# Optimization experiments

Hardware: AMD Instinct MI355X
Metric: run time of the kernel (lower is better)

The kernel has to match this reference:

```python
import jax, jax.numpy as jnp
import numpy as np

S, B, D = 2048, 2, 1024
H, DH = 16, 64  # heads, dim_head; H*DH == D (required by out.view)
SCALE = DH ** -0.5


def setup_inputs() -> dict:
    key = jax.random.key(0)
    ks = jax.random.split(key, 9)
    s = 0.02
    return {
        "x": jax.random.normal(ks[0], (S, B, D), jnp.float32),
        "Wq": jax.random.normal(ks[1], (H * DH, D), jnp.float32) * s,
        "bq": jax.random.normal(ks[2], (H * DH,), jnp.float32) * s,
        "Wk": jax.random.normal(ks[3], (H * DH, D), jnp.float32) * s,
        "bk": jax.random.normal(ks[4], (H * DH,), jnp.float32) * s,
        "Wv": jax.random.normal(ks[5], (H * DH, D), jnp.float32) * s,
        "bv": jax.random.normal(ks[6], (H * DH,), jnp.float32) * s,
        "Wo": jax.random.normal(ks[7], (D, H * DH), jnp.float32) * s,
        "bo": jax.random.normal(ks[8], (D,), jnp.float32) * s,
    }


def reference(x, Wq, bq, Wk, bk, Wv, bv, Wo, bo):
    # x: [S, B, D] (seq-first, matching the torch module)
    q = (x @ Wq.T + bq).reshape(S, B, H, DH)
    k = (x @ Wk.T + bk).reshape(S, B, H, DH)
    v = (x @ Wv.T + bv).reshape(S, B, H, DH)
    # scores: [B, H, S, S]
    dots = jnp.einsum("sbhd,tbhd->bhst", q, k) * SCALE
    attn = jax.nn.softmax(dots, axis=-1)  # dropout p=0.0 -> identity
    out = jnp.einsum("bhst,tbhd->sbhd", attn, v).reshape(S, B, H * DH)
    return out @ Wo.T + bo
```

## Files before the change

### kernel.cpp

```cpp
#include <hip/hip_runtime.h>
#include <hip/hip_bf16.h>

typedef unsigned short u16;
typedef unsigned int u32;
typedef __bf16 bf16x8 __attribute__((ext_vector_type(8)));
typedef float f32x4 __attribute__((ext_vector_type(4)));
typedef float f32x16 __attribute__((ext_vector_type(16)));

static constexpr int kS = 2048;
static constexpr int kB = 2;
static constexpr int kD = 1024;
static constexpr int kDH = 64;
static constexpr int kM = kS * kB;
static constexpr float kScale = 0.125f;
static constexpr float kLog2e = 1.44269504088896340736f;

__device__ __forceinline__ u16 f2bf(float f) {
  return __builtin_bit_cast(u16, static_cast<__bf16>(f));
}

__device__ __forceinline__ u32 pack2(float lo, float hi) {
  union { u16 h[2]; u32 u; } x;
  x.h[0] = f2bf(lo); x.h[1] = f2bf(hi);
  return x.u;
}

__device__ __forceinline__ void permswap(u32& a, u32& b) {
  asm volatile("v_permlane32_swap_b32 %0, %1" : "+v"(a), "+v"(b));
}

__device__ __forceinline__ float exp2_hw(float x) {
  float r;
  asm("v_exp_f32 %0, %1" : "=v"(r) : "v"(x));
  return r;
}

__device__ __forceinline__ void load_lds16(const void* g, void* l) {
  __builtin_amdgcn_global_load_lds(
      (const __attribute__((address_space(1))) void*)g,
      (__attribute__((address_space(3))) void*)l, 16, 0, 0);
}

__global__ void cast_f32_bf16(const float* __restrict__ in, u16* __restrict__ out, int n) {
  int i = (blockIdx.x * blockDim.x + threadIdx.x) * 4;
  const int stride = gridDim.x * blockDim.x * 4;
  for (; i < n; i += stride) {
    const float4 v = *reinterpret_cast<const float4*>(in + i);
    ushort4 o;
    o.x = f2bf(v.x); o.y = f2bf(v.y); o.z = f2bf(v.z); o.w = f2bf(v.w);
    *reinterpret_cast<ushort4*>(out + i) = o;
  }
}

__global__ void cast_w4(const float* __restrict__ Wq, const float* __restrict__ Wk,
                        const float* __restrict__ Wv, const float* __restrict__ Wo,
                        u16* __restrict__ dq, u16* __restrict__ dk,
                        u16* __restrict__ dv, u16* __restrict__ dw) {
  const float* src; u16* dst;
  switch (blockIdx.y) {
    case 0: src = Wq; dst = dq; break;
    case 1: src = Wk; dst = dk; break;
    case 2: src = Wv; dst = dv; break;
    default: src = Wo; dst = dw; break;
  }
  const int i = (blockIdx.x * blockDim.x + threadIdx.x) * 4;
  const float4 v = *reinterpret_cast<const float4*>(src + i);
  ushort4 o;
  o.x = f2bf(v.x); o.y = f2bf(v.y); o.z = f2bf(v.z); o.w = f2bf(v.w);
  *reinterpret_cast<ushort4*>(dst + i) = o;
}

template <int MODE>
__device__ __forceinline__ void gemm_body(
    const u16* __restrict__ A, const u16* __restrict__ W,
    const float* __restrict__ bias, void* __restrict__ Out,
    int M, int N, int K, float oscale) {
  __shared__ u16 As[128 * 32];
  __shared__ u16 Bs[128 * 32];
  const int tid = threadIdx.x;
  const int lane = tid & 63;
  const int wid = tid >> 6;
  const int wr = (wid >> 1) * 64;
  const int wc = (wid & 1) * 64;
  const int l15 = lane & 15;
  const int lg = lane >> 4;
  const int tm = blockIdx.x * 128;
  const int tn = blockIdx.y * 128;

  f32x4 acc[4][4] = {};

  for (int k0 = 0; k0 < K; k0 += 32) {
#pragma unroll
    for (int p = 0; p < 2; ++p) {
      const int c = p * 256 + tid;
      const int row = c >> 2;
      const int cc = c & 3;
      load_lds16(A + (size_t)(tm + row) * K + k0 + cc * 8, &As[c * 8]);
      load_lds16(W + (size_t)(tn + row) * K + k0 + cc * 8, &Bs[c * 8]);
    }
    __syncthreads();
    bf16x8 af[4], bw[4];
#pragma unroll
    for (int i = 0; i < 4; ++i) {
      af[i] = *reinterpret_cast<const bf16x8*>(&As[(wr + i * 16 + l15) * 32 + lg * 8]);
      bw[i] = *reinterpret_cast<const bf16x8*>(&Bs[(wc + i * 16 + l15) * 32 + lg * 8]);
    }
#pragma unroll
    for (int i = 0; i < 4; ++i)
#pragma unroll
      for (int j = 0; j < 4; ++j)
        acc[i][j] = __builtin_amdgcn_mfma_f32_16x16x32_bf16(af[i], bw[j], acc[i][j], 0, 0, 0);
    __syncthreads();
  }

#pragma unroll
  for (int i = 0; i < 4; ++i)
#pragma unroll
    for (int j = 0; j < 4; ++j)
#pragma unroll
      for (int r = 0; r < 4; ++r) {
        const int row = tm + wr + i * 16 + lg * 4 + r;
        const int col = tn + wc + j * 16 + l15;
        const float v = (acc[i][j][r] + bias[col]) * oscale;
        if constexpr (MODE == 0) {
          reinterpret_cast<u16*>(Out)[(size_t)row * N + col] = f2bf(v);
        } else if constexpr (MODE == 1) {
          reinterpret_cast<float*>(Out)[(size_t)row * N + col] = v;
        } else {
          const int s_ = row >> 1, b_ = row & 1;
          const int h_ = col >> 6, dh_ = col & 63;
          reinterpret_cast<u16*>(Out)[((size_t)(b_ * 16 + h_) * 64 + dh_) * kS + s_] = f2bf(v);
        }
      }
}

__global__ __launch_bounds__(256) void qkv_gemm(
    const u16* __restrict__ xb,
    const u16* __restrict__ Wqb, const u16* __restrict__ Wkb, const u16* __restrict__ Wvb,
    const float* __restrict__ bq, const float* __restrict__ bk, const float* __restrict__ bv,
    u16* __restrict__ Q, u16* __restrict__ K, u16* __restrict__ Vt) {
  const int z = blockIdx.z;
  if (z == 2) {
    gemm_body<2>(xb, Wvb, bv, Vt, kM, kD, kD, 1.0f);
  } else if (z == 0) {
    gemm_body<0>(xb, Wqb, bq, Q, kM, kD, kD, kScale * kLog2e);
  } else {
    gemm_body<0>(xb, Wkb, bk, K, kM, kD, kD, 1.0f);
  }
}

__global__ __launch_bounds__(256) void out_gemm(
    const u16* __restrict__ Ob, const u16* __restrict__ Wob,
    const float* __restrict__ bo, float* __restrict__ out) {
  gemm_body<1>(Ob, Wob, bo, out, kM, kD, kD, 1.0f);
}

__global__ __launch_bounds__(512, 4) void attn_fwd(
    const u16* __restrict__ Qg, const u16* __restrict__ Kg,
    const u16* __restrict__ Vtg, u16* __restrict__ Og) {
  __shared__ u16 Ksm[2][2][64 * 64];
  __shared__ u16 Vsm[2][2][64 * 64];

  const int tid = threadIdx.x;
  const int lane = tid & 63;
  const int w = tid >> 6;
  const int half = w >> 2;
  const int wsub = w & 3;
  const int ltid = tid & 255;
  const int l31 = lane & 31;
  const int hi = lane >> 5;

  const int bid = blockIdx.x;
  const int xcd = bid & 7;
  const int idx = bid >> 3;
  const int bh = xcd * 4 + (idx & 3);
  const int qb = idx >> 2;
  const int b = bh & 1;
  const int h = bh >> 1;
  const int hoff = h * kDH;
  const int vslot = b * 16 + h;
  const int qrow = qb * 128 + wsub * 32 + l31;

  bf16x8 qf[4];
#pragma unroll
  for (int ks = 0; ks < 4; ++ks)
    qf[ks] = *reinterpret_cast<const bf16x8*>(
        &Qg[(size_t)(qrow * kB + b) * kD + hoff + ks * 16 + hi * 8]);

  f32x16 acc[2] = {};
  float lac[4] = {0.f, 0.f, 0.f, 0.f};

  auto stage = [&](int t0, int buf) {
#pragma unroll
    for (int p = 0; p < 2; ++p) {
      const int c = p * 256 + ltid;
      const int row = c >> 3;
      const int cc = c & 7;
      const int scc = cc ^ (row & 7);
      load_lds16(&Kg[(size_t)((t0 + row) * kB + b) * kD + hoff + scc * 8],
                 &Ksm[half][buf][c * 8]);
      load_lds16(&Vtg[(size_t)(vslot * 64 + row) * kS + t0 + scc * 8],
                 &Vsm[half][buf][c * 8]);
    }
  };

  const int tbase = half * 16;
  stage(tbase * 64, 0);

#pragma unroll 1
  for (int ti = 0; ti < 16; ++ti) {
    asm volatile("s_waitcnt vmcnt(0)" ::: "memory");
    __builtin_amdgcn_sched_barrier(0);
    __builtin_amdgcn_s_barrier();
    __builtin_amdgcn_sched_barrier(0);
    if (ti + 1 < 16) stage((tbase + ti + 1) * 64, (ti + 1) & 1);

    const int cur = ti & 1;

    f32x16 sc[2] = {};
    __builtin_amdgcn_s_setprio(1);
#pragma unroll
    for (int nb = 0; nb < 2; ++nb) {
      const int krow = nb * 32 + l31;
#pragma unroll
      for (int ks = 0; ks < 4; ++ks) {
        const bf16x8 kf = *reinterpret_cast<const bf16x8*>(
            &Ksm[half][cur][krow * 64 + (((ks * 2 + hi) ^ (krow & 7)) * 8)]);
        sc[nb] = __builtin_amdgcn_mfma_f32_32x32x16_bf16(kf, qf[ks], sc[nb], 0, 0, 0);
      }
    }
    __builtin_amdgcn_s_setprio(0);

    bf16x8 pb[4];
#pragma unroll
    for (int nb = 0; nb < 2; ++nb) {
      float p[16];
#pragma unroll
      for (int r = 0; r < 16; ++r) {
        p[r] = exp2_hw(sc[nb][r]);
        lac[r & 3] += p[r];
      }
      u32 pk[4][2];
#pragma unroll
      for (int q = 0; q < 4; ++q)
#pragma unroll
        for (int w2 = 0; w2 < 2; ++w2)
          pk[q][w2] = pack2(p[4 * q + 2 * w2], p[4 * q + 2 * w2 + 1]);
#pragma unroll
      for (int k1 = 0; k1 < 2; ++k1) {
        u32 a0 = pk[2 * k1][0], b0 = pk[2 * k1 + 1][0];
        u32 a1 = pk[2 * k1][1], b1 = pk[2 * k1 + 1][1];
        permswap(a0, b0);
        permswap(a1, b1);
        union { u32 wv[4]; bf16x8 v; } U;
        U.wv[0] = a0; U.wv[1] = a1; U.wv[2] = b0; U.wv[3] = b1;
        pb[2 * nb + k1] = U.v;
      }
    }

    __builtin_amdgcn_s_setprio(1);
#pragma unroll
    for (int ks = 0; ks < 4; ++ks)
#pragma unroll
      for (int n2 = 0; n2 < 2; ++n2) {
        const int vrow = n2 * 32 + l31;
        const bf16x8 va = *reinterpret_cast<const bf16x8*>(
            &Vsm[half][cur][vrow * 64 + (((ks * 2 + hi) ^ (vrow & 7)) * 8)]);
        acc[n2] = __builtin_amdgcn_mfma_f32_32x32x16_bf16(va, pb[ks], acc[n2], 0, 0, 0);
      }
    __builtin_amdgcn_s_setprio(0);
  }

  __syncthreads();
  float* Ocmb = reinterpret_cast<float*>(&Ksm[0][0][0]);
  float* Lcmb = reinterpret_cast<float*>(&Vsm[0][0][0]);
  const float l_own = (lac[0] + lac[1]) + (lac[2] + lac[3]);
  const float l_half = l_own + __shfl_xor(l_own, 32);
  const int q = wsub * 32 + l31;

  if (half == 1) {
    if (hi == 0) Lcmb[q] = l_half;
#pragma unroll
    for (int n2 = 0; n2 < 2; ++n2)
#pragma unroll
      for (int q4 = 0; q4 < 4; ++q4)
#pragma unroll
        for (int rp = 0; rp < 2; ++rp) {
          const int dh0 = n2 * 32 + q4 * 8 + hi * 4 + rp * 2;
          const int a = q * 64 + (dh0 ^ ((l31 & 7) << 3));
          *reinterpret_cast<float2*>(&Ocmb[a]) =
              make_float2(acc[n2][q4 * 4 + rp * 2], acc[n2][q4 * 4 + rp * 2 + 1]);
        }
  }
  __syncthreads();
  if (half == 0) {
    const float inv = 1.0f / (l_half + Lcmb[q]);
#pragma unroll
    for (int n2 = 0; n2 < 2; ++n2)
#pragma unroll
      for (int q4 = 0; q4 < 4; ++q4)
#pragma unroll
        for (int rp = 0; rp < 2; ++rp) {
          const int dh0 = n2 * 32 + q4 * 8 + hi * 4 + rp * 2;
          const int a = q * 64 + (dh0 ^ ((l31 & 7) << 3));
          const float2 o = *reinterpret_cast<const float2*>(&Ocmb[a]);
          acc[n2][q4 * 4 + rp * 2]     += o.x;
          acc[n2][q4 * 4 + rp * 2 + 1] += o.y;
        }
#pragma unroll
    for (int n2 = 0; n2 < 2; ++n2)
#pragma unroll
      for (int g = 0; g < 4; ++g) {
        const int dh0 = n2 * 32 + g * 8 + hi * 4;
        ushort4 o;
        o.x = f2bf(acc[n2][g * 4 + 0] * inv);
        o.y = f2bf(acc[n2][g * 4 + 1] * inv);
        o.z = f2bf(acc[n2][g * 4 + 2] * inv);
        o.w = f2bf(acc[n2][g * 4 + 3] * inv);
        *reinterpret_cast<ushort4*>(&Og[(size_t)(qrow * kB + b) * kD + hoff + dh0]) = o;
      }
  }
}

extern "C" void kernel_launch(void* const* d_in, const int* in_sizes, int n_in,
                              void* d_out, int out_size, void* d_ws, size_t ws_size,
                              hipStream_t stream) {
  const float* x  = (const float*)d_in[0];
  const float* Wq = (const float*)d_in[1];
  const float* bq = (const float*)d_in[2];
  const float* Wk = (const float*)d_in[3];
  const float* bk = (const float*)d_in[4];
  const float* Wv = (const float*)d_in[5];
  const float* bv = (const float*)d_in[6];
  const float* Wo = (const float*)d_in[7];
  const float* bo = (const float*)d_in[8];
  float* out = (float*)d_out;

  char* ws = (char*)d_ws;
  u16* xb  = (u16*)(ws + 0);
  u16* Wqb = (u16*)(ws + 8388608);
  u16* Wkb = (u16*)(ws + 10485760);
  u16* Wvb = (u16*)(ws + 12582912);
  u16* Wob = (u16*)(ws + 14680064);
  u16* Qb  = (u16*)(ws + 16777216);
  u16* Kb  = (u16*)(ws + 25165824);
  u16* Vtb = (u16*)(ws + 33554432);
  u16* Ob  = (u16*)(ws + 41943040);

  cast_f32_bf16<<<4096, 256, 0, stream>>>(x, xb, kM * kD);
  cast_w4<<<dim3(1024, 4), 256, 0, stream>>>(Wq, Wk, Wv, Wo, Wqb, Wkb, Wvb, Wob);

  qkv_gemm<<<dim3(kM / 128, kD / 128, 3), 256, 0, stream>>>(
      xb, Wqb, Wkb, Wvb, bq, bk, bv, Qb, Kb, Vtb);

  attn_fwd<<<512, 512, 0, stream>>>(Qb, Kb, Vtb, Ob);

  out_gemm<<<dim3(kM / 128, kD / 128), 256, 0, stream>>>(Ob, Wob, bo, out);
}
```

Measured before the change: 132.4 us.

## Triple-buffer GEMM LDS tiles with async prefetch two steps ahead

Replaces the single-buffered GEMM k-loop with a three-stage LDS ring. Global-to-LDS loads for step k+2 are issued while step k computes. Manual vmcnt waits and a single barrier per iteration replace the two __syncthreads, so memory latency overlaps with MFMA work. This triples LDS use, which may lower occupancy. It also depends on load_lds16 issuing exactly the counted number of vector memory ops.

```diff
diff --git a/kernel.cpp b/kernel.cpp
--- a/kernel.cpp
+++ b/kernel.cpp
@@ -75,8 +75,8 @@
     const u16* __restrict__ A, const u16* __restrict__ W,
     const float* __restrict__ bias, void* __restrict__ Out,
     int M, int N, int K, float oscale) {
-  __shared__ u16 As[128 * 32];
-  __shared__ u16 Bs[128 * 32];
+  __shared__ u16 As[3][128 * 32];
+  __shared__ u16 Bs[3][128 * 32];
   const int tid = threadIdx.x;
   const int lane = tid & 63;
   const int wid = tid >> 6;
@@ -87,30 +87,45 @@
   const int tm = blockIdx.x * 128;
   const int tn = blockIdx.y * 128;
 
-  f32x4 acc[4][4] = {};
-
-  for (int k0 = 0; k0 < K; k0 += 32) {
+  auto stage = [&](int k0, int buf) {
 #pragma unroll
     for (int p = 0; p < 2; ++p) {
       const int c = p * 256 + tid;
       const int row = c >> 2;
       const int cc = c & 3;
-      load_lds16(A + (size_t)(tm + row) * K + k0 + cc * 8, &As[c * 8]);
-      load_lds16(W + (size_t)(tn + row) * K + k0 + cc * 8, &Bs[c * 8]);
-    }
-    __syncthreads();
+      load_lds16(A + (size_t)(tm + row) * K + k0 + cc * 8, &As[buf][c * 8]);
+      load_lds16(W + (size_t)(tn + row) * K + k0 + cc * 8, &Bs[buf][c * 8]);
+    }
+  };
+
+  f32x4 acc[4][4] = {};
+  const int nsteps = K / 32;
+
+  stage(0, 0);
+  stage(32, 1);
+
+#pragma unroll 1
+  for (int ks = 0; ks < nsteps; ++ks) {
+    if (ks < nsteps - 1) asm volatile("s_waitcnt vmcnt(4)" ::: "memory");
+    else                 asm volatile("s_waitcnt vmcnt(0)" ::: "memory");
+    __builtin_amdgcn_sched_barrier(0);
+    __builtin_amdgcn_s_barrier();
+    __builtin_amdgcn_sched_barrier(0);
+    if (ks + 2 < nsteps) stage((ks + 2) * 32, (ks + 2) % 3);
+
+    const u16* as = As[ks % 3];
+    const u16* bs = Bs[ks % 3];
     bf16x8 af[4], bw[4];
 #pragma unroll
     for (int i = 0; i < 4; ++i) {
-      af[i] = *reinterpret_cast<const bf16x8*>(&As[(wr + i * 16 + l15) * 32 + lg * 8]);
-      bw[i] = *reinterpret_cast<const bf16x8*>(&Bs[(wc + i * 16 + l15) * 32 + lg * 8]);
+      af[i] = *reinterpret_cast<const bf16x8*>(&as[(wr + i * 16 + l15) * 32 + lg * 8]);
+      bw[i] = *reinterpret_cast<const bf16x8*>(&bs[(wc + i * 16 + l15) * 32 + lg * 8]);
     }
 #pragma unroll
     for (int i = 0; i < 4; ++i)
 #pragma unroll
       for (int j = 0; j < 4; ++j)
         acc[i][j] = __builtin_amdgcn_mfma_f32_16x16x32_bf16(af[i], bw[j], acc[i][j], 0, 0, 0);
-    __syncthreads();
   }
 
 #pragma unroll
```

Measured after the change: 148.2 us. +12.0%, slower.

## Use 512-thread GEMM blocks with K=64 stages and XOR-swizzled LDS

Applied to the files above, without the earlier changes.

The shared GEMM body used by the QKV and output projections now runs 8 waves per block instead of 4, each wave owning a 64x32 output tile. Each stage loads a K-slice of 64 instead of 32, which halves the number of barriers per K loop. The LDS tiles use an XOR swizzle on 16-byte chunks to avoid bank conflicts on the fragment reads. The intent is more latency hiding and fewer synchronizations per unit of work, at the cost of more LDS per block and fewer accumulator tiles per wave, which lowers per-wave reuse.

```diff
diff --git a/kernel.cpp b/kernel.cpp
--- a/kernel.cpp
+++ b/kernel.cpp
@@ -75,48 +75,63 @@
     const u16* __restrict__ A, const u16* __restrict__ W,
     const float* __restrict__ bias, void* __restrict__ Out,
     int M, int N, int K, float oscale) {
-  __shared__ u16 As[128 * 32];
-  __shared__ u16 Bs[128 * 32];
+  __shared__ u16 As[128 * 64];
+  __shared__ u16 Bs[128 * 64];
   const int tid = threadIdx.x;
   const int lane = tid & 63;
   const int wid = tid >> 6;
-  const int wr = (wid >> 1) * 64;
-  const int wc = (wid & 1) * 64;
+  const int wr = (wid >> 2) * 64;
+  const int wc = (wid & 3) * 32;
   const int l15 = lane & 15;
   const int lg = lane >> 4;
   const int tm = blockIdx.x * 128;
   const int tn = blockIdx.y * 128;
 
-  f32x4 acc[4][4] = {};
-
-  for (int k0 = 0; k0 < K; k0 += 32) {
+  auto stage = [&](int k0) {
 #pragma unroll
     for (int p = 0; p < 2; ++p) {
-      const int c = p * 256 + tid;
-      const int row = c >> 2;
-      const int cc = c & 3;
-      load_lds16(A + (size_t)(tm + row) * K + k0 + cc * 8, &As[c * 8]);
-      load_lds16(W + (size_t)(tn + row) * K + k0 + cc * 8, &Bs[c * 8]);
-    }
+      const int c = p * 512 + tid;
+      const int row = c >> 3;
+      const int scc = (c & 7) ^ (row & 7);
+      load_lds16(A + (size_t)(tm + row) * K + k0 + scc * 8, &As[c * 8]);
+      load_lds16(W + (size_t)(tn + row) * K + k0 + scc * 8, &Bs[c * 8]);
+    }
+  };
+
+  f32x4 acc[4][2] = {};
+
+#pragma unroll 1
+  for (int ks = 0; ks < K / 64; ++ks) {
+    stage(ks * 64);
     __syncthreads();
-    bf16x8 af[4], bw[4];
-#pragma unroll
-    for (int i = 0; i < 4; ++i) {
-      af[i] = *reinterpret_cast<const bf16x8*>(&As[(wr + i * 16 + l15) * 32 + lg * 8]);
-      bw[i] = *reinterpret_cast<const bf16x8*>(&Bs[(wc + i * 16 + l15) * 32 + lg * 8]);
-    }
-#pragma unroll
-    for (int i = 0; i < 4; ++i)
-#pragma unroll
-      for (int j = 0; j < 4; ++j)
-        acc[i][j] = __builtin_amdgcn_mfma_f32_16x16x32_bf16(af[i], bw[j], acc[i][j], 0, 0, 0);
+#pragma unroll
+    for (int kh = 0; kh < 2; ++kh) {
+      bf16x8 af[4], bw[2];
+#pragma unroll
+      for (int i = 0; i < 4; ++i) {
+        const int row = wr + i * 16 + l15;
+        af[i] = *reinterpret_cast<const bf16x8*>(
+            &As[row * 64 + (((kh * 4 + lg) ^ (row & 7)) * 8)]);
+      }
+#pragma unroll
+      for (int j = 0; j < 2; ++j) {
+        const int row = wc + j * 16 + l15;
+        bw[j] = *reinterpret_cast<const bf16x8*>(
+            &Bs[row * 64 + (((kh * 4 + lg) ^ (row & 7)) * 8)]);
+      }
+#pragma unroll
+      for (int i = 0; i < 4; ++i)
+#pragma unroll
+        for (int j = 0; j < 2; ++j)
+          acc[i][j] = __builtin_amdgcn_mfma_f32_16x16x32_bf16(af[i], bw[j], acc[i][j], 0, 0, 0);
+    }
     __syncthreads();
   }
 
 #pragma unroll
   for (int i = 0; i < 4; ++i)
 #pragma unroll
-    for (int j = 0; j < 4; ++j)
+    for (int j = 0; j < 2; ++j)
 #pragma unroll
       for (int r = 0; r < 4; ++r) {
         const int row = tm + wr + i * 16 + lg * 4 + r;
@@ -134,7 +149,7 @@
       }
 }
 
-__global__ __launch_bounds__(256) void qkv_gemm(
+__global__ __launch_bounds__(512, 6) void qkv_gemm(
     const u16* __restrict__ xb,
     const u16* __restrict__ Wqb, const u16* __restrict__ Wkb, const u16* __restrict__ Wvb,
     const float* __restrict__ bq, const float* __restrict__ bk, const float* __restrict__ bv,
@@ -149,7 +164,7 @@
   }
 }
 
-__global__ __launch_bounds__(256) void out_gemm(
+__global__ __launch_bounds__(512, 6) void out_gemm(
     const u16* __restrict__ Ob, const u16* __restrict__ Wob,
     const float* __restrict__ bo, float* __restrict__ out) {
   gemm_body<1>(Ob, Wob, bo, out, kM, kD, kD, 1.0f);
@@ -350,10 +365,10 @@
   cast_f32_bf16<<<4096, 256, 0, stream>>>(x, xb, kM * kD);
   cast_w4<<<dim3(1024, 4), 256, 0, stream>>>(Wq, Wk, Wv, Wo, Wqb, Wkb, Wvb, Wob);
 
-  qkv_gemm<<<dim3(kM / 128, kD / 128, 3), 256, 0, stream>>>(
+  qkv_gemm<<<dim3(kM / 128, kD / 128, 3), 512, 0, stream>>>(
       xb, Wqb, Wkb, Wvb, bq, bk, bv, Qb, Kb, Vtb);
 
   attn_fwd<<<512, 512, 0, stream>>>(Qb, Kb, Vtb, Ob);
 
-  out_gemm<<<dim3(kM / 128, kD / 128), 256, 0, stream>>>(Ob, Wob, bo, out);
-}
+  out_gemm<<<dim3(kM / 128, kD / 128), 512, 0, stream>>>(Ob, Wob, bo, out);
+}
```

Result: faster. 118.3 us (-10.7%).
